# Kernel optimization log

Hardware: AMD Instinct MI355X
Metric: run time of the kernel (lower is better)

## Reference

```python
import jax, jax.numpy as jnp
import numpy as np
import math

IN_CH = 512
OUT_CH = 512
KSIZE = 3
W_DIM = 512
CONV_SCALE = 1.0 / math.sqrt(IN_CH * KSIZE * KSIZE)
MOD_SCALE = 1.0 / math.sqrt(W_DIM)


def setup_inputs() -> dict:
    key = jax.random.key(0)
    k1, k2, k3, k4 = jax.random.split(key, 4)
    B, H, W = 16, 64, 64
    return {
        "input": jax.random.normal(k1, (B, IN_CH, H, W), dtype=jnp.float32),
        "style": jax.random.normal(k2, (B, W_DIM), dtype=jnp.float32),
        "weight": jax.random.normal(k3, (1, OUT_CH, IN_CH, KSIZE, KSIZE), dtype=jnp.float32),
        "mod_weight": jax.random.normal(k4, (IN_CH, W_DIM), dtype=jnp.float32),
        "mod_bias": jnp.ones((IN_CH,), dtype=jnp.float32),
    }


def reference(input, style, weight, mod_weight, mod_bias):
    B, Cin, H, Wd = input.shape
    # EqualLinear modulation: style -> per-sample, per-input-channel scale
    s = style @ (mod_weight * MOD_SCALE).T + mod_bias  # [B, Cin]
    s = s[:, None, :, None, None]                      # [B,1,Cin,1,1]
    w = CONV_SCALE * weight * s                        # [B,Cout,Cin,k,k]
    demod = jax.lax.rsqrt(jnp.sum(w * w, axis=(2, 3, 4)) + 1e-8)  # [B,Cout]
    w = w * demod[:, :, None, None, None]
    # Grouped conv with groups=batch, same as torch F.conv2d
    w = w.reshape(B * OUT_CH, Cin, KSIZE, KSIZE)
    x = input.reshape(1, B * Cin, H, Wd)
    pad = KSIZE // 2
    out = jax.lax.conv_general_dilated(
        x, w,
        window_strides=(1, 1),
        padding=[(pad, pad), (pad, pad)],
        dimension_numbers=("NCHW", "OIHW", "NCHW"),
        feature_group_count=B,
    )
    return out.reshape(B, OUT_CH, out.shape[2], out.shape[3])
```

## Files before the change

### kernel.cpp

```cpp
#include <hip/hip_runtime.h>
#include <hip/hip_bf16.h>


constexpr float CONV_SCALE = 0.014731391274719738f;
constexpr float MOD_SCALE  = 0.04419417382415922f;

typedef short  bf16x8 __attribute__((ext_vector_type(8)));
typedef float  f32x4  __attribute__((ext_vector_type(4)));

__device__ __forceinline__ unsigned short f2bf(float f) {
  unsigned u = __float_as_uint(f);
  u += 0x7fffu + ((u >> 16) & 1u);
  return (unsigned short)(u >> 16);
}

__device__ __forceinline__ void async16(const void* g, void* l) {
  __builtin_amdgcn_global_load_lds((const __attribute__((address_space(1))) unsigned int*)g,
                                   (__attribute__((address_space(3))) unsigned int*)l,
                                   16, 0, 0);
}

__global__ void k_style(const float* __restrict__ style, const float* __restrict__ mw,
                        const float* __restrict__ mb, float* __restrict__ s) {
  int t = blockIdx.x * 256 + threadIdx.x;
  int b = t & 15, i = t >> 4;
  const float4* st = (const float4*)(style + b * 512);
  const float4* wr = (const float4*)(mw + i * 512);
  float acc = 0.f;
#pragma unroll 8
  for (int j = 0; j < 128; ++j) {
    float4 a = st[j], w4 = wr[j];
    acc += a.x * w4.x + a.y * w4.y + a.z * w4.z + a.w * w4.w;
  }
  s[b * 512 + i] = acc * MOD_SCALE + mb[i];
}

__global__ void k_prepw(const float* __restrict__ w, float* __restrict__ wsq,
                        unsigned short* __restrict__ wt) {
  __shared__ float Wl[2304];
  int t = threadIdx.x;
  size_t base = (size_t)blockIdx.x * 2304;
#pragma unroll
  for (int k = 0; k < 3; ++k) {
    int idx = t + k * 256;
    if (idx < 576) ((float4*)Wl)[idx] = ((const float4*)(w + base))[idx];
  }
  __syncthreads();
  int g = blockIdx.x * 256 + t;
  int ic = g & 511, o = g >> 9;
  float ssq = 0.f;
#pragma unroll
  for (int tap = 0; tap < 9; ++tap) {
    float v = Wl[t * 9 + tap];
    ssq += v * v;
    wt[((size_t)tap * 512 + o) * 512 + ic] = f2bf(v);
  }
  wsq[o * 512 + ic] = ssq;
}

__global__ void k_dscale(const float* __restrict__ s, const float* __restrict__ wsq,
                         float* __restrict__ dscale) {
  int t = blockIdx.x * 256 + threadIdx.x;
  int b = t & 15, o = t >> 4;
  const float4* sq = (const float4*)(wsq + o * 512);
  const float4* sb = (const float4*)(s + b * 512);
  float acc = 0.f;
#pragma unroll 8
  for (int j = 0; j < 128; ++j) {
    float4 q4 = sq[j], s4 = sb[j];
    acc += q4.x * s4.x * s4.x + q4.y * s4.y * s4.y + q4.z * s4.z * s4.z + q4.w * s4.w * s4.w;
  }
  float d = rsqrtf(CONV_SCALE * CONV_SCALE * acc + 1e-8f);
  dscale[b * 512 + o] = d * CONV_SCALE;
}

__global__ void k_zpad(unsigned short* __restrict__ xt) {
  int strip = blockIdx.x;
  int b = strip >> 1, sel = strip & 1;
  unsigned short* p = xt + ((size_t)(b * 66 + sel * 65) * 64) * 512;
  int4 z = {0, 0, 0, 0};
  for (int idx = threadIdx.x; idx < 4096; idx += 256)
    ((int4*)p)[idx] = z;
}

__global__ void k_xt(const float* __restrict__ x, const float* __restrict__ s,
                     unsigned short* __restrict__ xt) {
  __shared__ float T[64][68];
  int h = blockIdx.x, b = blockIdx.y;
  const float* xp = x + (size_t)b * 512 * 4096 + h * 64;
  unsigned short* xo = xt + ((size_t)((b * 66) + h + 1) * 64) * 512;
  int t = threadIdx.x;
  for (int ic0 = 0; ic0 < 512; ic0 += 64) {
#pragma unroll
    for (int k = 0; k < 4; ++k) {
      int idx = t + k * 256;
      int icl = idx >> 4, c4 = idx & 15;
      int ic = ic0 + icl;
      float4 v = *(const float4*)&xp[(size_t)ic * 4096 + c4 * 4];
      float sc = s[b * 512 + ic];
      v.x *= sc; v.y *= sc; v.z *= sc; v.w *= sc;
      *(float4*)&T[icl][(c4 ^ (icl >> 3)) << 2] = v;
    }
    __syncthreads();
#pragma unroll
    for (int c = t; c < 512; c += 256) {
      int wv = c >> 3, ig = (c & 7) * 8;
      int colf = ((((c >> 3) >> 2) ^ (c & 7)) << 2) + ((c >> 3) & 3);
      unsigned p0 = (unsigned)f2bf(T[ig + 0][colf]) | ((unsigned)f2bf(T[ig + 1][colf]) << 16);
      unsigned p1 = (unsigned)f2bf(T[ig + 2][colf]) | ((unsigned)f2bf(T[ig + 3][colf]) << 16);
      unsigned p2 = (unsigned)f2bf(T[ig + 4][colf]) | ((unsigned)f2bf(T[ig + 5][colf]) << 16);
      unsigned p3 = (unsigned)f2bf(T[ig + 6][colf]) | ((unsigned)f2bf(T[ig + 7][colf]) << 16);
      uint4 pk = {p0, p1, p2, p3};
      *(uint4*)&xo[(size_t)wv * 512 + ic0 + ig] = pk;
    }
    __syncthreads();
  }
}

__global__ __launch_bounds__(512, 2)
void k_conv(const unsigned short* __restrict__ xt, const unsigned short* __restrict__ wt,
            const float* __restrict__ dscale, float* __restrict__ out) {
  __shared__ short Xs[2][10 * 66 * 32];
  __shared__ short Ws[2][3 * 128 * 32];

  const int b  = blockIdx.z;
  const int o0 = blockIdx.y * 128;
  const int h0 = blockIdx.x * 8;
  const int t = threadIdx.x;
  const int wave = t >> 6, lane = t & 63;
  const int q = lane >> 4, l16 = lane & 15;

  const int xsrc8 = ((lane & 3) ^ ((((lane >> 2) + 1) >> 1) & 3)) * 8;
  const int wsrc8 = ((lane & 3) ^ ((lane >> 3) & 3)) * 8;
  const int wq8 = (q ^ ((l16 >> 1) & 3)) * 8;

  f32x4 acc[8][4];
#pragma unroll
  for (int i = 0; i < 8; ++i)
#pragma unroll
    for (int j = 0; j < 4; ++j) acc[i][j] = (f32x4){0.f, 0.f, 0.f, 0.f};

  for (int z = t; z < 640; z += 512) {
    int bi = (z >= 320) ? 1 : 0;
    int zz = z - bi * 320;
    int r = zz >> 5, rem = zz & 31;
    int col = (rem >> 4) * 65, ch2 = (rem & 15) * 2;
    *(int*)&Xs[bi][(r * 66 + col) * 32 + ch2] = 0;
  }

  auto stageX = [&](int i_, int xb_) {
    int ic0_ = i_ * 32;
#pragma unroll
    for (int j = 0; j < 5; ++j) {
      int c = wave * 5 + j;
      int row = c >> 2, q16 = c & 3;
      async16(xt + ((size_t)((b * 66 + h0 + row) * 64) + q16 * 16 + (lane >> 2)) * 512 + ic0_ + xsrc8,
              &Xs[xb_][(row * 66 + 1 + q16 * 16) * 32]);
    }
  };
  auto stageW = [&](int i_, int kh_, int wb_) {
    int ic0_ = i_ * 32;
#pragma unroll
    for (int j = 0; j < 3; ++j) {
      int ci = wave * 3 + j;
      int kw = ci >> 3, oo = ((ci & 7) << 4) + (lane >> 2);
      async16(wt + (((size_t)(kh_ * 3 + kw) * 512 + o0 + oo) * 512 + ic0_ + wsrc8),
              &Ws[wb_][ci * 512]);
    }
  };
  auto compute = [&](int kh, int xb_, int wb_) {
    const short* Xrow = &Xs[xb_][(wave + kh) * 66 * 32];
    const short* Wb = Ws[wb_];
    __builtin_amdgcn_s_setprio(1);
#pragma unroll
    for (int kw = 0; kw < 3; ++kw) {
      bf16x8 bfr[4];
#pragma unroll
      for (int ni = 0; ni < 4; ++ni) {
        int c = ni * 16 + l16 + kw;
        bfr[ni] = *(const bf16x8*)&Xrow[c * 32 + ((q ^ ((c >> 1) & 3)) << 3)];
      }
#pragma unroll
      for (int mi = 0; mi < 8; ++mi) {
        bf16x8 af = *(const bf16x8*)&Wb[(kw * 128 + mi * 16 + l16) * 32 + wq8];
#pragma unroll
        for (int ni = 0; ni < 4; ++ni)
          acc[mi][ni] = __builtin_amdgcn_mfma_f32_16x16x32_bf16(af, bfr[ni], acc[mi][ni], 0, 0, 0);
      }
    }
    __builtin_amdgcn_s_setprio(0);
  };

  stageX(0, 0);
  stageW(0, 0, 0);
  __syncthreads();

#pragma unroll 2
  for (int i = 0; i < 16; ++i) {
    const int xb = i & 1;
    const int inext = (i < 15) ? i + 1 : 15;
    stageW(i, 1, xb ^ 1);
    stageX(inext, xb ^ 1);
    asm volatile("s_waitcnt vmcnt(8)" ::: "memory");
    __builtin_amdgcn_s_barrier();
    __builtin_amdgcn_sched_barrier(0);
    compute(0, xb, xb);
    __builtin_amdgcn_sched_barrier(0);
    __builtin_amdgcn_s_barrier();
    stageW(i, 2, xb);
    asm volatile("s_waitcnt vmcnt(8)" ::: "memory");
    __builtin_amdgcn_s_barrier();
    __builtin_amdgcn_sched_barrier(0);
    compute(1, xb, xb ^ 1);
    __builtin_amdgcn_sched_barrier(0);
    __builtin_amdgcn_s_barrier();
    stageW(inext, 0, xb ^ 1);
    asm volatile("s_waitcnt vmcnt(3)" ::: "memory");
    __builtin_amdgcn_s_barrier();
    __builtin_amdgcn_sched_barrier(0);
    compute(2, xb, xb);
    __builtin_amdgcn_sched_barrier(0);
    __builtin_amdgcn_s_barrier();
  }
  asm volatile("s_waitcnt vmcnt(0)" ::: "memory");

  const int h = h0 + wave;
#pragma unroll
  for (int mi = 0; mi < 8; ++mi) {
#pragma unroll
    for (int r = 0; r < 4; ++r) {
      int o_l = mi * 16 + q * 4 + r;
      float ds = dscale[b * 512 + o0 + o_l];
      float* orow = out + ((size_t)(b * 512 + o0 + o_l) * 64 + h) * 64;
#pragma unroll
      for (int ni = 0; ni < 4; ++ni)
        orow[ni * 16 + l16] = acc[mi][ni][r] * ds;
    }
  }
}

extern "C" void kernel_launch(void* const* d_in, const int* in_sizes, int n_in,
                              void* d_out, int out_size, void* d_ws, size_t ws_size,
                              hipStream_t stream) {
  const float* x      = (const float*)d_in[0];
  const float* style  = (const float*)d_in[1];
  const float* weight = (const float*)d_in[2];
  const float* mw     = (const float*)d_in[3];
  const float* mb     = (const float*)d_in[4];
  float* out = (float*)d_out;

  float* s      = (float*)d_ws;
  float* dscale = s + 8192;
  float* wsq    = dscale + 8192;
  unsigned short* wt = (unsigned short*)(wsq + 262144);
  unsigned short* xt = wt + 9 * 512 * 512;

  k_style<<<32, 256, 0, stream>>>(style, mw, mb, s);
  k_prepw<<<1024, 256, 0, stream>>>(weight, wsq, wt);
  k_dscale<<<32, 256, 0, stream>>>(s, wsq, dscale);
  k_zpad<<<32, 256, 0, stream>>>(xt);
  k_xt<<<dim3(64, 16), 256, 0, stream>>>(x, s, xt);
  k_conv<<<dim3(8, 4, 16), 512, 0, stream>>>(xt, wt, dscale, out);
}
```

Measured before the change: 526.7 us.

## Enlarge per-wave conv tile, triple-buffer weights, and remove LDS transpose in k_xt

```diff
diff --git a/kernel.cpp b/kernel.cpp
--- a/kernel.cpp
+++ b/kernel.cpp
@@ -85,47 +85,45 @@
 
 __global__ void k_xt(const float* __restrict__ x, const float* __restrict__ s,
                      unsigned short* __restrict__ xt) {
-  __shared__ float T[64][68];
   int h = blockIdx.x, b = blockIdx.y;
   const float* xp = x + (size_t)b * 512 * 4096 + h * 64;
-  unsigned short* xo = xt + ((size_t)((b * 66) + h + 1) * 64) * 512;
+  unsigned short* xo = xt + ((size_t)(b * 66 + h + 1) * 64) * 512;
   int t = threadIdx.x;
-  for (int ic0 = 0; ic0 < 512; ic0 += 64) {
-#pragma unroll
-    for (int k = 0; k < 4; ++k) {
-      int idx = t + k * 256;
-      int icl = idx >> 4, c4 = idx & 15;
-      int ic = ic0 + icl;
-      float4 v = *(const float4*)&xp[(size_t)ic * 4096 + c4 * 4];
-      float sc = s[b * 512 + ic];
-      v.x *= sc; v.y *= sc; v.z *= sc; v.w *= sc;
-      *(float4*)&T[icl][(c4 ^ (icl >> 3)) << 2] = v;
-    }
-    __syncthreads();
-#pragma unroll
-    for (int c = t; c < 512; c += 256) {
-      int wv = c >> 3, ig = (c & 7) * 8;
-      int colf = ((((c >> 3) >> 2) ^ (c & 7)) << 2) + ((c >> 3) & 3);
-      unsigned p0 = (unsigned)f2bf(T[ig + 0][colf]) | ((unsigned)f2bf(T[ig + 1][colf]) << 16);
-      unsigned p1 = (unsigned)f2bf(T[ig + 2][colf]) | ((unsigned)f2bf(T[ig + 3][colf]) << 16);
-      unsigned p2 = (unsigned)f2bf(T[ig + 4][colf]) | ((unsigned)f2bf(T[ig + 5][colf]) << 16);
-      unsigned p3 = (unsigned)f2bf(T[ig + 6][colf]) | ((unsigned)f2bf(T[ig + 7][colf]) << 16);
-      uint4 pk = {p0, p1, p2, p3};
-      *(uint4*)&xo[(size_t)wv * 512 + ic0 + ig] = pk;
-    }
-    __syncthreads();
-  }
-}
-
-__global__ __launch_bounds__(512, 2)
+  int o8 = t >> 4, wq = t & 15;
+  for (int ic0 = 0; ic0 < 512; ic0 += 128) {
+    int icb = ic0 + o8 * 8;
+    float4 v[8];
+    float sc[8];
+#pragma unroll
+    for (int r = 0; r < 8; ++r) {
+      v[r] = *(const float4*)&xp[(size_t)(icb + r) * 4096 + wq * 4];
+      sc[r] = s[b * 512 + icb + r];
+    }
+#pragma unroll
+    for (int j = 0; j < 4; ++j) {
+      unsigned pk[4];
+#pragma unroll
+      for (int p = 0; p < 4; ++p) {
+        float lo = ((const float*)&v[2 * p])[j]     * sc[2 * p];
+        float hi = ((const float*)&v[2 * p + 1])[j] * sc[2 * p + 1];
+        pk[p] = (unsigned)f2bf(lo) | ((unsigned)f2bf(hi) << 16);
+      }
+      *(uint4*)&xo[(size_t)(wq * 4 + j) * 512 + icb] = *(uint4*)pk;
+    }
+  }
+}
+
+__global__ __launch_bounds__(256, 1)
 void k_conv(const unsigned short* __restrict__ xt, const unsigned short* __restrict__ wt,
             const float* __restrict__ dscale, float* __restrict__ out) {
   __shared__ short Xs[2][10 * 66 * 32];
-  __shared__ short Ws[2][3 * 128 * 32];
-
-  const int b  = blockIdx.z;
-  const int o0 = blockIdx.y * 128;
-  const int h0 = blockIdx.x * 8;
+  __shared__ short Wb[3][3 * 128 * 32];
+
+  const int lin = blockIdx.x;
+  const int k8 = lin & 7, jj = lin >> 3;
+  const int o0 = (k8 >> 1) * 128;
+  const int b  = ((k8 & 1) << 3) | (jj >> 3);
+  const int h0 = (jj & 7) * 8;
   const int t = threadIdx.x;
   const int wave = t >> 6, lane = t & 63;
   const int q = lane >> 4, l16 = lane & 15;
@@ -134,13 +132,13 @@
   const int wsrc8 = ((lane & 3) ^ ((lane >> 3) & 3)) * 8;
   const int wq8 = (q ^ ((l16 >> 1) & 3)) * 8;
 
-  f32x4 acc[8][4];
+  f32x4 acc[8][8];
 #pragma unroll
   for (int i = 0; i < 8; ++i)
 #pragma unroll
-    for (int j = 0; j < 4; ++j) acc[i][j] = (f32x4){0.f, 0.f, 0.f, 0.f};
-
-  for (int z = t; z < 640; z += 512) {
+    for (int j = 0; j < 8; ++j) acc[i][j] = (f32x4){0.f, 0.f, 0.f, 0.f};
+
+  for (int z = t; z < 640; z += 256) {
     int bi = (z >= 320) ? 1 : 0;
     int zz = z - bi * 320;
     int r = zz >> 5, rem = zz & 31;
@@ -151,8 +149,8 @@
   auto stageX = [&](int i_, int xb_) {
     int ic0_ = i_ * 32;
 #pragma unroll
-    for (int j = 0; j < 5; ++j) {
-      int c = wave * 5 + j;
+    for (int j2 = 0; j2 < 10; ++j2) {
+      int c = wave * 10 + j2;
       int row = c >> 2, q16 = c & 3;
       async16(xt + ((size_t)((b * 66 + h0 + row) * 64) + q16 * 16 + (lane >> 2)) * 512 + ic0_ + xsrc8,
               &Xs[xb_][(row * 66 + 1 + q16 * 16) * 32]);
@@ -161,31 +159,32 @@
   auto stageW = [&](int i_, int kh_, int wb_) {
     int ic0_ = i_ * 32;
 #pragma unroll
-    for (int j = 0; j < 3; ++j) {
-      int ci = wave * 3 + j;
+    for (int j2 = 0; j2 < 6; ++j2) {
+      int ci = wave * 6 + j2;
       int kw = ci >> 3, oo = ((ci & 7) << 4) + (lane >> 2);
       async16(wt + (((size_t)(kh_ * 3 + kw) * 512 + o0 + oo) * 512 + ic0_ + wsrc8),
-              &Ws[wb_][ci * 512]);
+              &Wb[wb_][ci * 512]);
     }
   };
-  auto compute = [&](int kh, int xb_, int wb_) {
-    const short* Xrow = &Xs[xb_][(wave + kh) * 66 * 32];
-    const short* Wb = Ws[wb_];
+  auto compute = [&](int kh, int cur) {
     __builtin_amdgcn_s_setprio(1);
 #pragma unroll
     for (int kw = 0; kw < 3; ++kw) {
-      bf16x8 bfr[4];
-#pragma unroll
-      for (int ni = 0; ni < 4; ++ni) {
-        int c = ni * 16 + l16 + kw;
-        bfr[ni] = *(const bf16x8*)&Xrow[c * 32 + ((q ^ ((c >> 1) & 3)) << 3)];
-      }
+      bf16x8 bfr[8];
+#pragma unroll
+      for (int rr = 0; rr < 2; ++rr)
+#pragma unroll
+        for (int ni = 0; ni < 4; ++ni) {
+          int c = ni * 16 + l16 + kw;
+          bfr[rr * 4 + ni] = *(const bf16x8*)
+              &Xs[cur][((2 * wave + kh + rr) * 66 + c) * 32 + ((q ^ ((c >> 1) & 3)) << 3)];
+        }
 #pragma unroll
       for (int mi = 0; mi < 8; ++mi) {
-        bf16x8 af = *(const bf16x8*)&Wb[(kw * 128 + mi * 16 + l16) * 32 + wq8];
-#pragma unroll
-        for (int ni = 0; ni < 4; ++ni)
-          acc[mi][ni] = __builtin_amdgcn_mfma_f32_16x16x32_bf16(af, bfr[ni], acc[mi][ni], 0, 0, 0);
+        bf16x8 af = *(const bf16x8*)&Wb[kh][(kw * 128 + mi * 16 + l16) * 32 + wq8];
+#pragma unroll
+        for (int nj = 0; nj < 8; ++nj)
+          acc[mi][nj] = __builtin_amdgcn_mfma_f32_16x16x32_bf16(af, bfr[nj], acc[mi][nj], 0, 0, 0);
       }
     }
     __builtin_amdgcn_s_setprio(0);
@@ -193,50 +192,44 @@
 
   stageX(0, 0);
   stageW(0, 0, 0);
+  stageW(0, 1, 1);
   __syncthreads();
 
 #pragma unroll 2
   for (int i = 0; i < 16; ++i) {
-    const int xb = i & 1;
-    const int inext = (i < 15) ? i + 1 : 15;
-    stageW(i, 1, xb ^ 1);
-    stageX(inext, xb ^ 1);
-    asm volatile("s_waitcnt vmcnt(8)" ::: "memory");
+    const int cur = i & 1;
+    const int inx = (i < 15) ? i + 1 : 15;
+    stageW(i, 2, 2);
+    stageX(inx, cur ^ 1);
+    compute(0, cur);
+    asm volatile("s_waitcnt vmcnt(16)" ::: "memory");
     __builtin_amdgcn_s_barrier();
-    __builtin_amdgcn_sched_barrier(0);
-    compute(0, xb, xb);
-    __builtin_amdgcn_sched_barrier(0);
+    stageW(inx, 0, 0);
+    compute(1, cur);
+    asm volatile("s_waitcnt vmcnt(16)" ::: "memory");
     __builtin_amdgcn_s_barrier();
-    stageW(i, 2, xb);
-    asm volatile("s_waitcnt vmcnt(8)" ::: "memory");
+    stageW(inx, 1, 1);
+    compute(2, cur);
+    asm volatile("s_waitcnt vmcnt(6)" ::: "memory");
     __builtin_amdgcn_s_barrier();
-    __builtin_amdgcn_sched_barrier(0);
-    compute(1, xb, xb ^ 1);
-    __builtin_amdgcn_sched_barrier(0);
-    __builtin_amdgcn_s_barrier();
-    stageW(inext, 0, xb ^ 1);
-    asm volatile("s_waitcnt vmcnt(3)" ::: "memory");
-    __builtin_amdgcn_s_barrier();
-    __builtin_amdgcn_sched_barrier(0);
-    compute(2, xb, xb);
-    __builtin_amdgcn_sched_barrier(0);
-    __builtin_amdgcn_s_barrier();
   }
   asm volatile("s_waitcnt vmcnt(0)" ::: "memory");
 
-  const int h = h0 + wave;
-#pragma unroll
-  for (int mi = 0; mi < 8; ++mi) {
+#pragma unroll
+  for (int mi = 0; mi < 8; ++mi)
 #pragma unroll
     for (int r = 0; r < 4; ++r) {
       int o_l = mi * 16 + q * 4 + r;
       float ds = dscale[b * 512 + o0 + o_l];
-      float* orow = out + ((size_t)(b * 512 + o0 + o_l) * 64 + h) * 64;
-#pragma unroll
-      for (int ni = 0; ni < 4; ++ni)
-        orow[ni * 16 + l16] = acc[mi][ni][r] * ds;
-    }
-  }
+#pragma unroll
+      for (int rr = 0; rr < 2; ++rr) {
+        int h = h0 + 2 * wave + rr;
+        float* orow = out + ((size_t)(b * 512 + o0 + o_l) * 64 + h) * 64;
+#pragma unroll
+        for (int ni = 0; ni < 4; ++ni)
+          orow[ni * 16 + l16] = acc[mi][rr * 4 + ni][r] * ds;
+      }
+    }
 }
 
 extern "C" void kernel_launch(void* const* d_in, const int* in_sizes, int n_in,
@@ -260,5 +253,5 @@
   k_dscale<<<32, 256, 0, stream>>>(s, wsq, dscale);
   k_zpad<<<32, 256, 0, stream>>>(xt);
   k_xt<<<dim3(64, 16), 256, 0, stream>>>(x, s, xt);
-  k_conv<<<dim3(8, 4, 16), 512, 0, stream>>>(xt, wt, dscale, out);
-}
+  k_conv<<<512, 256, 0, stream>>>(xt, wt, dscale, out);
+}
```

Result: slower. 843.1 us (+60.1%).
